# Performance work log

Hardware: AMD Instinct MI355X
Metric: run time of the kernel (lower is better)

Reference implementation:

```python
import jax, jax.numpy as jnp
import numpy as np
import math

# Static config (mirrors init_kwargs)
E, B, S, D, F, HMAX = 8, 4, 1024, 1024, 4096, 8
W = 768                      # active slimmable width (multiple giving integer head_dim)
H = max(1, W * HMAX // D)    # = 6 heads at width 768
HD = W // H                  # = 128
TOPK = 2
EPS = 1e-6


def setup_inputs() -> dict:
    key = jax.random.key(0)
    ks = jax.random.split(key, 14)
    sd = 1.0 / math.sqrt(D)
    sf = 1.0 / math.sqrt(F)
    return {
        "x":  jax.random.normal(ks[0], (B, S, D), jnp.float32),
        "wr": jax.random.normal(ks[1], (D, E), jnp.float32) * sd,
        "qw": jax.random.normal(ks[2], (E, D, D), jnp.float32) * sd,
        "qb": jax.random.normal(ks[3], (E, D), jnp.float32) * sd,
        "kw": jax.random.normal(ks[4], (E, D, D), jnp.float32) * sd,
        "kb": jax.random.normal(ks[5], (E, D), jnp.float32) * sd,
        "vw": jax.random.normal(ks[6], (E, D, D), jnp.float32) * sd,
        "vb": jax.random.normal(ks[7], (E, D), jnp.float32) * sd,
        "ow": jax.random.normal(ks[8], (E, D, D), jnp.float32) * sd,
        "ob": jax.random.normal(ks[9], (E, D), jnp.float32) * sd,
        "w1": jax.random.normal(ks[10], (E, F, D), jnp.float32) * sd,
        "b1": jax.random.normal(ks[11], (E, F), jnp.float32) * sd,
        "w2": jax.random.normal(ks[12], (E, D, F), jnp.float32) * sf,
        "b2": jax.random.normal(ks[13], (E, D), jnp.float32) * sf,
    }


def _slim_linear(x, w, b, in_w, out_w):
    # SlimmableLinear: dynamically slice max-size weight/bias to active widths
    return x @ w[:out_w, :in_w].T + b[:out_w]


def _rms_norm(x):
    # SlimmableExpert._layer_norm: RMS normalization (no mean-subtract, no affine)
    var = jnp.mean(jnp.square(x), axis=-1, keepdims=True)
    return x / jnp.sqrt(var + EPS)


def _expert_fwd(x_s, qw, qb, kw, kb, vw, vb, ow, ob, w1, b1, w2, b2):
    # x_s: [B, S, W]  (already sliced to active width)
    # --- slimmable self-attention at width W ---
    q = _slim_linear(x_s, qw, qb, W, W).reshape(B, S, H, HD).transpose(0, 2, 1, 3)
    k = _slim_linear(x_s, kw, kb, W, W).reshape(B, S, H, HD).transpose(0, 2, 1, 3)
    v = _slim_linear(x_s, vw, vb, W, W).reshape(B, S, H, HD).transpose(0, 2, 1, 3)
    scores = jnp.einsum('bhqd,bhkd->bhqk', q, k) / math.sqrt(HD)   # [B,H,S,S]
    attn = jax.nn.softmax(scores, axis=-1)
    ao = jnp.einsum('bhqk,bhkd->bhqd', attn, v)
    ao = ao.transpose(0, 2, 1, 3).reshape(B, S, W)
    ao = _slim_linear(ao, ow, ob, W, W)
    x1 = _rms_norm(x_s + ao)
    # --- slimmable FFN: W -> F (full) -> W, exact GELU (torch default) ---
    h = jax.nn.gelu(_slim_linear(x1, w1, b1, W, F), approximate=False)
    f = _slim_linear(h, w2, b2, F, W)
    return _rms_norm(x1 + f)   # [B,S,W]


def reference(x, wr, qw, qb, kw, kb, vw, vb, ow, ob, w1, b1, w2, b2):
    # Router: softmax over experts, top-k dispatch with renormalized gates
    logits = jnp.einsum('bsd,de->bse', x, wr)            # [B,S,E]
    probs = jax.nn.softmax(logits, axis=-1)
    topv, topi = jax.lax.top_k(probs, TOPK)              # [B,S,K]
    topv = topv / jnp.sum(topv, axis=-1, keepdims=True)
    bi = jnp.arange(B)[:, None, None]
    si = jnp.arange(S)[None, :, None]
    gate = jnp.zeros((B, S, E), x.dtype).at[bi, si, topi].set(topv)  # sparse gate

    # Slice tokens to active width (width embedding skipped: closest stored
    # width 736 != 768, per source shape-match check)
    x_s = x[..., :W]
    outs = []
    for e in range(E):   # small fixed expert count; bounds peak memory
        outs.append(_expert_fwd(x_s, qw[e], qb[e], kw[e], kb[e], vw[e], vb[e],
                                ow[e], ob[e], w1[e], b1[e], w2[e], b2[e]))
    eo = jnp.stack(outs, axis=0)                          # [E,B,S,W]
    out_w = jnp.einsum('bse,ebsw->bsw', gate, eo)         # gate-weighted combine
    # Zero-pad sliced width back to full model dim (per SlimmableExpert)
    out = jnp.concatenate(
        [out_w, jnp.zeros((B, S, D - W), x.dtype)], axis=-1)
    return out
```

## Files before the change

kernel.cpp:

```cpp
#include <hip/hip_runtime.h>
#include <cstdint>

#define NE 8
#define NB 4
#define NS 1024
#define ND 1024
#define NF 4096
#define NW 768
#define NH 6
#define NHD 128
#define NTOK 4096
#define NBH 24
#define RCAP 10496
#define VSTRIDE ((size_t)NTOK * NW)
#define EPS 1e-6f

typedef unsigned short ush;
typedef __attribute__((ext_vector_type(8))) short short8;
typedef __attribute__((ext_vector_type(4))) float f32x4;
typedef __attribute__((ext_vector_type(4))) unsigned short u16x4;

typedef const __attribute__((address_space(1))) void gvoid_t;
typedef __attribute__((address_space(3))) void lvoid_t;

__device__ __forceinline__ void gload16(const void* g, void* l) {
  __builtin_amdgcn_global_load_lds((gvoid_t*)g, (lvoid_t*)l, 16, 0, 0);
}

__device__ __forceinline__ ush f2b(float f) {
  union { float f; uint32_t u; } x; x.f = f;
  uint32_t r = x.u + 0x7fffu + ((x.u >> 16) & 1u);
  return (ush)(r >> 16);
}
__device__ __forceinline__ float b2f(ush u) {
  union { uint32_t u; float f; } x; x.u = (uint32_t)u << 16;
  return x.f;
}
__device__ __forceinline__ int prefix_sum(const int* __restrict__ c, int n) {
  int s = 0;
#pragma unroll 1
  for (int i = 0; i < n; ++i) s += c[i];
  return s;
}


__global__ __launch_bounds__(256, 4)
void router_kernel(const float* __restrict__ x, const float* __restrict__ wr,
                   float* __restrict__ gate, int* __restrict__ inv) {
  int lane = threadIdx.x & 63, wave = threadIdx.x >> 6;
  int t = blockIdx.x * 4 + wave;
  float acc[NE] = {};
  for (int i = 0; i < 16; ++i) {
    int d = lane + i * 64;
    float xv = x[(size_t)t * ND + d];
    const float* wp = wr + (size_t)d * NE;
    float4 w0 = *(const float4*)wp, w1 = *(const float4*)(wp + 4);
    acc[0] += xv * w0.x; acc[1] += xv * w0.y; acc[2] += xv * w0.z; acc[3] += xv * w0.w;
    acc[4] += xv * w1.x; acc[5] += xv * w1.y; acc[6] += xv * w1.z; acc[7] += xv * w1.w;
  }
#pragma unroll
  for (int e = 0; e < NE; ++e)
    for (int m = 1; m < 64; m <<= 1) acc[e] += __shfl_xor(acc[e], m);
  int i1 = 0; float v1 = acc[0];
#pragma unroll
  for (int e = 1; e < NE; ++e) if (acc[e] > v1) { v1 = acc[e]; i1 = e; }
  int i2 = -1; float v2 = -3.0e38f;
#pragma unroll
  for (int e = 0; e < NE; ++e) if (e != i1 && acc[e] > v2) { v2 = acc[e]; i2 = e; }
  float p2 = __expf(v2 - v1);
  float g1 = 1.0f / (1.0f + p2), g2 = p2 / (1.0f + p2);
  if (lane < NE)
    gate[(size_t)t * NE + lane] = (lane == i1) ? g1 : ((lane == i2) ? g2 : 0.0f);
  if (lane < 2) inv[t * 2 + lane] = -1;
}

__global__ __launch_bounds__(1024, 1)
void build_index(const float* __restrict__ gate, int* __restrict__ cnt64s,
                 int* __restrict__ idx_all, int* __restrict__ inv) {
  int e = blockIdx.x >> 2, b = blockIdx.x & 3;
  int s = threadIdx.x, t = b * 1024 + s;
  bool on = gate[(size_t)t * NE + e] > 0.0f;
  idx_all[(e * 4 + b) * 1024 + s] = (b * 1024) | (int)0x80000000;
  __shared__ int wsum[16], wbase[16];
  unsigned long long mask = __ballot(on);
  int lane = s & 63, wv = s >> 6;
  if (lane == 0) wsum[wv] = __popcll(mask);
  __syncthreads();
  if (s == 0) {
    int acc = 0;
    for (int i = 0; i < 16; ++i) { wbase[i] = acc; acc += wsum[i]; }
    cnt64s[e * 4 + b] = (acc + 63) & ~63;
  }
  __syncthreads();
  if (on) {
    int pos = wbase[wv] + __popcll(mask & ((1ull << lane) - 1ull));
    idx_all[(e * 4 + b) * 1024 + pos] = t;
    int k = 0;
#pragma unroll
    for (int j = 0; j < NE; ++j) k += (j < e && gate[(size_t)t * NE + j] > 0.0f);
    inv[t * 2 + k] = (e << 12) | pos;
  }
}

__global__ __launch_bounds__(256, 4)
void cast_all(const float* __restrict__ x,
              const float* __restrict__ qw, const float* __restrict__ kw,
              const float* __restrict__ vw, const float* __restrict__ ow,
              const float* __restrict__ w1, const float* __restrict__ w2,
              ush* __restrict__ xs,
              ush* __restrict__ dq, ush* __restrict__ dk, ush* __restrict__ dv,
              ush* __restrict__ dwo, ush* __restrict__ d1, ush* __restrict__ d2) {
  int y = blockIdx.y;
  if (y == 8) {
    const int n4 = NTOK * NW / 4;
    for (int u = blockIdx.x * 256 + threadIdx.x; u < n4; u += gridDim.x * 256) {
      int r = u / (NW / 4), c = u - r * (NW / 4);
      float4 v = *(const float4*)(x + (size_t)r * ND + c * 4);
      u16x4 o; o.x = f2b(v.x); o.y = f2b(v.y); o.z = f2b(v.z); o.w = f2b(v.w);
      *(u16x4*)(xs + (size_t)u * 4) = o;
    }
    return;
  }
  const int e = y;
  const int Q4 = 147456;
  const int W14 = 786432;
  const int total = 4 * Q4 + 2 * W14;
  const float* qe = qw + (size_t)e * ND * ND;
  const float* ke = kw + (size_t)e * ND * ND;
  const float* ve = vw + (size_t)e * ND * ND;
  const float* oe = ow + (size_t)e * ND * ND;
  const float* w1e = w1 + (size_t)e * NF * ND;
  const float* w2e = w2 + (size_t)e * ND * NF;
  ush* dqe = dq + (size_t)e * NW * NW;
  ush* dke = dk + (size_t)e * NW * NW;
  ush* dve = dv + (size_t)e * NW * NW;
  ush* doe = dwo + (size_t)e * NW * NW;
  ush* d1e = d1 + (size_t)e * NF * NW;
  ush* d2e = d2 + (size_t)e * NW * NF;
  for (int u = blockIdx.x * 256 + threadIdx.x; u < total; u += gridDim.x * 256) {
    const float* src; ush* dst; int ldsrc, cols4, rel;
    if (u < 4 * Q4) {
      int which = u / Q4; rel = u - which * Q4;
      src = (which == 0) ? qe : (which == 1) ? ke : (which == 2) ? ve : oe;
      dst = (which == 0) ? dqe : (which == 1) ? dke : (which == 2) ? dve : doe;
      ldsrc = 1024; cols4 = 192;
    } else if (u < 4 * Q4 + W14) {
      rel = u - 4 * Q4; src = w1e; dst = d1e; ldsrc = 1024; cols4 = 192;
    } else {
      rel = u - 4 * Q4 - W14; src = w2e; dst = d2e; ldsrc = 4096; cols4 = 1024;
    }
    int r = rel / cols4, c = rel - r * cols4;
    float4 v = *(const float4*)(src + (size_t)r * ldsrc + (size_t)c * 4);
    u16x4 o; o.x = f2b(v.x); o.y = f2b(v.y); o.z = f2b(v.z); o.w = f2b(v.w);
    *(u16x4*)(dst + (size_t)rel * 4) = o;
  }
}

#define BM 128
#define BN 128

__device__ __forceinline__ float gelu_fast(float v) {
  float u = v * fmaf(0.0356774081f, v * v, 0.7978845608f);
  float p = __expf(2.0f * fabsf(u));
  float th = fmaf(-2.0f, __builtin_amdgcn_rcpf(p + 1.0f), 1.0f);
  th = copysignf(th, u);
  return 0.5f * v * (1.0f + th);
}

__device__ __forceinline__ void stage_geom2(int tid, int u, int PAIR, int& row, int& kb) {
  row = u + PAIR * (((tid >> 2) ^ (u >> 2)) & 1);
  kb = ((tid ^ u) & 3) << 4;
}

__global__ __launch_bounds__(256, 3)
void qkv_gemm(const ush* __restrict__ A,
              const ush* __restrict__ wqb, const ush* __restrict__ wkb,
              const ush* __restrict__ wvb,
              const float* __restrict__ qbias, const float* __restrict__ kbias,
              const float* __restrict__ vbias,
              ush* __restrict__ qg, ush* __restrict__ kg, ush* __restrict__ vtg,
              const int* __restrict__ cnt64s, const int* __restrict__ idx_all) {
  const int bid = blockIdx.x;
  const int e = bid & 7, wi = bid >> 3;
  const int bn = wi % 6, bm = (wi / 6) % 32, w = wi / 192;
  int sb = 0, cnt = 0;
  if (w == 0) {
    int sec = e * 4 + (bm >> 3);
    cnt = cnt64s[sec];
    if (((bm & 7) * 128) >= cnt) return;
    sb = prefix_sum(cnt64s, sec);
  }
  const ush* Bw = ((w == 0) ? wqb : (w == 1) ? wkb : wvb) + (size_t)e * NW * NW;
  const float* bias = ((w == 0) ? qbias : (w == 1) ? kbias : vbias) + (size_t)e * ND;

  __shared__ __align__(16) char LDS[3 * 16384];

  const int tid = threadIdx.x, lane = tid & 63, wave = tid >> 6;
  const int lr = lane & 15, lg = lane >> 4;
  const int wr = wave >> 1, wc = wave & 1;

  size_t srcOff[4];
#pragma unroll
  for (int c = 0; c < 4; ++c) {
    int u = (c & 1) * 32 + (tid >> 3), row, kb;
    stage_geom2(tid, u, 64, row, kb);
    int gRow;
    if (c < 2) {
      if (w == 0) {
        int lrow = (bm & 7) * 128 + row;
        gRow = idx_all[(e * 4 + (bm >> 3)) * 1024 + lrow] & 0x7fffffff;
      } else {
        gRow = bm * BM + row;
      }
    } else {
      gRow = bn * BN + row;
    }
    srcOff[c] = (size_t)gRow * (NW * 2) + kb;
  }

  int offA[4], offB[4];
#pragma unroll
  for (int i = 0; i < 4; ++i) {
    offA[i] = (i * 16 + lr) * 128 + (((wr << 6) | (lg << 4)) ^ ((lr & 7) << 4));
    offB[i] = (i * 16 + lr) * 128 + (((wc << 6) | (lg << 4)) ^ ((lr & 7) << 4)) + 8192;
  }

  auto stg = [&](int slot, int kt) {
    size_t kOff = (size_t)kt * 64;
    char* dst = LDS + slot * 16384;
#pragma unroll
    for (int c = 0; c < 4; ++c) {
      const char* src = (c < 2) ? (const char*)A + srcOff[c] + kOff
                                : (const char*)Bw + srcOff[c] + kOff;
      gload16(src, dst + c * 4096 + tid * 16);
    }
  };

  f32x4 acc[4][4] = {};
  const int nkt = NW / 32;
  stg(0, 0); stg(1, 1);
  asm volatile("s_waitcnt vmcnt(4)" ::: "memory");
  asm volatile("s_barrier" ::: "memory");
  int slot = 0;
  for (int kt = 0; kt < nkt; ++kt) {
    int s2 = slot + 2; if (s2 >= 3) s2 -= 3;
    bool more = (kt + 2 < nkt);
    if (more) stg(s2, kt + 2);
    const char* base = LDS + slot * 16384;
    short8 af[4], bfr[4];
#pragma unroll
    for (int i = 0; i < 4; ++i) {
      af[i] = *(const short8*)(base + offA[i]);
      bfr[i] = *(const short8*)(base + offB[i]);
    }
    __builtin_amdgcn_s_setprio(1);
#pragma unroll
    for (int i = 0; i < 4; ++i)
#pragma unroll
      for (int j = 0; j < 4; ++j)
        acc[i][j] = __builtin_amdgcn_mfma_f32_16x16x32_bf16(af[i], bfr[j], acc[i][j], 0, 0, 0);
    __builtin_amdgcn_s_setprio(0);
    if (more) asm volatile("s_waitcnt vmcnt(4)" ::: "memory");
    else      asm volatile("s_waitcnt vmcnt(0)" ::: "memory");
    asm volatile("s_barrier" ::: "memory");
    slot = (slot == 2) ? 0 : slot + 1;
  }

  if (w == 2) {
#pragma unroll
    for (int i = 0; i < 4; ++i) {
      int sl = wr * 64 + i * 16 + lg * 4;
#pragma unroll
      for (int j = 0; j < 4; ++j) {
        int d = wc * 64 + j * 16 + lr;
        float bb = bias[bn * BN + d];
        u16x4 wv_;
#pragma unroll
        for (int r = 0; r < 4; ++r) wv_[r] = f2b(acc[i][j][r] + bb);
        *(u16x4*)(LDS + d * 256 + ((sl * 2) ^ ((d & 15) << 4))) = wv_;
      }
    }
    __syncthreads();
    int d = tid >> 1, sh = (tid & 1) * 64;
    int b_ = bm >> 3, s0b = (bm & 7) * 128;
    ush* gdst = vtg + (size_t)e * VSTRIDE +
                ((size_t)(b_ * NH + bn) * NHD + d) * NS + s0b + sh;
#pragma unroll
    for (int c = 0; c < 8; ++c) {
      short8 v = *(const short8*)(LDS + d * 256 + (((sh + c * 8) * 2) ^ ((d & 15) << 4)));
      *(short8*)(gdst + c * 8) = v;
    }
    return;
  }

#pragma unroll
  for (int i = 0; i < 4; ++i) {
    int lm16 = (bm & 7) * 128 + wr * 64 + i * 16;
    int m0 = bm * BM + wr * 64 + i * 16 + lg * 4;
#pragma unroll
    for (int j = 0; j < 4; ++j) {
      int n = bn * BN + wc * 64 + j * 16 + lr;
      float bb = bias[n];
      if (w == 0) {
        if (lm16 < cnt) {
          int grow = sb + lm16 + lg * 4;
#pragma unroll
          for (int r = 0; r < 4; ++r)
            qg[(size_t)(grow + r) * NW + n] = f2b(acc[i][j][r] + bb);
        }
      } else {
        ush* o = kg + (size_t)e * NTOK * NW;
#pragma unroll
        for (int r = 0; r < 4; ++r)
          o[(size_t)(m0 + r) * NW + n] = f2b(acc[i][j][r] + bb);
      }
    }
  }
}

__global__ __launch_bounds__(256, 3)
void attn2(const ush* __restrict__ Qg, const ush* __restrict__ Kg,
           const ush* __restrict__ VTg, ush* __restrict__ ao,
           const int* __restrict__ cnt64s) {
  const int bid = blockIdx.x;
  const int e = bid & 7, wi = bid >> 3;
  const int qb = wi & 15, bh = wi >> 4;
  const int b = bh / NH, h = bh % NH;
  const int sec = e * 4 + b;
  const int cnt = cnt64s[sec];
  if (qb * 64 >= cnt) return;
  const int sb = prefix_sum(cnt64s, sec);

  __shared__ __align__(16) ush Ks[64 * 128];
  __shared__ __align__(16) ush VTs[128 * 64];
  __shared__ __align__(16) ush Ps[4 * 16 * 64];

  const int tid = threadIdx.x, lane = tid & 63, wave = tid >> 6;
  const int lr = lane & 15, lg = lane >> 4;
  const float cexp = 1.4426950408889634f / sqrtf((float)NHD);

  const ush* Ke = Kg + (size_t)e * NTOK * NW;
  const ush* Ve = VTg + (size_t)e * VSTRIDE;

  int growq = sb + qb * 64 + wave * 16 + lr;
  short8 qf[4];
#pragma unroll
  for (int kk = 0; kk < 4; ++kk)
    qf[kk] = *(const short8*)(Qg + (size_t)growq * NW + h * NHD + kk * 32 + lg * 8);

  f32x4 accv[8] = {};
  float mr[4] = {-3.0e38f, -3.0e38f, -3.0e38f, -3.0e38f};
  float ls[4] = {};

  for (int kt = 0; kt < 16; ++kt) {
    __syncthreads();
#pragma unroll
    for (int p = 0; p < 4; ++p) {
      int o = p * 4096 + tid * 16;
      int row = o >> 8, cb = o & 255;
      gload16((const char*)Ke + ((size_t)(b * NS + kt * 64 + row) * NW + h * NHD) * 2 +
                  (cb ^ ((row & 7) << 4)),
              (char*)Ks + o);
    }
#pragma unroll
    for (int p = 0; p < 4; ++p) {
      int o = p * 4096 + tid * 16;
      int d = o >> 7, cb = o & 127;
      gload16((const char*)Ve + ((size_t)((b * NH + h) * NHD + d) * NS + kt * 64) * 2 +
                  (cb ^ ((d & 7) << 4)),
              (char*)VTs + o);
    }
    __syncthreads();

    f32x4 s[4] = {};
    __builtin_amdgcn_s_setprio(1);
#pragma unroll
    for (int kg2 = 0; kg2 < 4; ++kg2)
#pragma unroll
      for (int kk = 0; kk < 4; ++kk) {
        int row = kg2 * 16 + lr;
        short8 kf = *(const short8*)((const char*)Ks + row * 256 +
                                     ((kk * 64 + lg * 16) ^ ((row & 7) << 4)));
        s[kg2] = __builtin_amdgcn_mfma_f32_16x16x32_bf16(qf[kk], kf, s[kg2], 0, 0, 0);
      }
    __builtin_amdgcn_s_setprio(0);

    float mt[4];
#pragma unroll
    for (int r = 0; r < 4; ++r) {
      float m0 = fmaxf(fmaxf(s[0][r], s[1][r]), fmaxf(s[2][r], s[3][r]));
#pragma unroll
      for (int mm = 1; mm < 16; mm <<= 1) m0 = fmaxf(m0, __shfl_xor(m0, mm));
      mt[r] = m0;
    }
    bool need = (mt[0] > mr[0] + 8.f) || (mt[1] > mr[1] + 8.f) ||
                (mt[2] > mr[2] + 8.f) || (mt[3] > mr[3] + 8.f);
    if (__any(need)) {
#pragma unroll
      for (int r = 0; r < 4; ++r) {
        float mn = fmaxf(mr[r], mt[r]);
        float sc = exp2f((mr[r] - mn) * cexp);
        mr[r] = mn; ls[r] *= sc;
#pragma unroll
        for (int dg = 0; dg < 8; ++dg) accv[dg][r] *= sc;
      }
    }

    char* pw = (char*)Ps + wave * 2048;
#pragma unroll
    for (int kg2 = 0; kg2 < 4; ++kg2)
#pragma unroll
      for (int r = 0; r < 4; ++r) {
        float p = exp2f((s[kg2][r] - mr[r]) * cexp);
        ls[r] += p;
        int row = lg * 4 + r;
        *(ush*)(pw + row * 128 + (((kg2 * 16 + lr) * 2) ^ ((row & 7) << 4))) = f2b(p);
      }
    short8 pf[2];
#pragma unroll
    for (int kk2 = 0; kk2 < 2; ++kk2)
      pf[kk2] = *(const short8*)(pw + lr * 128 + ((kk2 * 64 + lg * 16) ^ ((lr & 7) << 4)));

    __builtin_amdgcn_s_setprio(1);
#pragma unroll
    for (int dg = 0; dg < 8; ++dg) {
      int d = dg * 16 + lr;
#pragma unroll
      for (int kk2 = 0; kk2 < 2; ++kk2) {
        short8 vf = *(const short8*)((const char*)VTs + d * 128 +
                                     ((kk2 * 64 + lg * 16) ^ ((d & 7) << 4)));
        accv[dg] = __builtin_amdgcn_mfma_f32_16x16x32_bf16(pf[kk2], vf, accv[dg], 0, 0, 0);
      }
    }
    __builtin_amdgcn_s_setprio(0);
  }

#pragma unroll
  for (int r = 0; r < 4; ++r)
#pragma unroll
    for (int mm = 1; mm < 16; mm <<= 1) ls[r] += __shfl_xor(ls[r], mm);

#pragma unroll
  for (int r = 0; r < 4; ++r) {
    int growr = sb + qb * 64 + wave * 16 + lg * 4 + r;
    float inv_ = 1.0f / ls[r];
#pragma unroll
    for (int dg = 0; dg < 8; ++dg)
      ao[(size_t)growr * NW + h * NHD + dg * 16 + lr] = f2b(accv[dg][r] * inv_);
  }
}

__global__ __launch_bounds__(256, 2)
void csr_gemm_w(const ush* __restrict__ A, const ush* __restrict__ Ball,
                const float* __restrict__ biasAll, ush* __restrict__ out,
                int N, int Kld, int klen, int nbn,
                int strideBe, int biasStride,
                const int* __restrict__ cnt64s) {
  const int bid = blockIdx.x;
  const int e = bid & 7, wi = bid >> 3;
  const int bn = wi % nbn, bm = wi / nbn;
  const int Re = cnt64s[e * 4] + cnt64s[e * 4 + 1] + cnt64s[e * 4 + 2] + cnt64s[e * 4 + 3];
  if (bm * BM >= Re) return;
  const int ebase = prefix_sum(cnt64s, e * 4);
  const ush* Bw = Ball + (size_t)e * strideBe;
  const float* bias = biasAll + (size_t)e * biasStride;

  __shared__ __align__(16) char LDS[3 * 24576];

  const int tid = threadIdx.x, lane = tid & 63, wave = tid >> 6;
  const int lr = lane & 15, lg = lane >> 4;
  const int wr = wave >> 1, wc = wave & 1;

  size_t srcOff[6];
#pragma unroll
  for (int c = 0; c < 2; ++c) {
    int u = c * 32 + (tid >> 3), row, kb;
    stage_geom2(tid, u, 64, row, kb);
    srcOff[c] = (size_t)(ebase + bm * BM + row) * (Kld * 2) + kb;
  }
#pragma unroll
  for (int c = 0; c < 4; ++c) {
    int u = c * 32 + (tid >> 3), row, kb;
    stage_geom2(tid, u, 128, row, kb);
    srcOff[2 + c] = (size_t)(bn * 256 + row) * (Kld * 2) + kb;
  }

  int offA[4], offB[8];
#pragma unroll
  for (int i = 0; i < 4; ++i)
    offA[i] = (i * 16 + lr) * 128 + (((wr << 6) | (lg << 4)) ^ ((lr & 7) << 4));
#pragma unroll
  for (int j = 0; j < 8; ++j)
    offB[j] = (j * 16 + lr) * 128 + (((wc << 6) | (lg << 4)) ^ ((lr & 7) << 4)) + 8192;

  auto stg = [&](int slot, int kt) {
    size_t kOff = (size_t)kt * 64;
    char* dst = LDS + slot * 24576;
#pragma unroll
    for (int c = 0; c < 2; ++c)
      gload16((const char*)A + srcOff[c] + kOff, dst + c * 4096 + tid * 16);
#pragma unroll
    for (int c = 0; c < 4; ++c)
      gload16((const char*)Bw + srcOff[2 + c] + kOff, dst + 8192 + c * 4096 + tid * 16);
  };

  f32x4 acc[4][8] = {};
  const int nkt = klen / 32;
  stg(0, 0); stg(1, 1);
  asm volatile("s_waitcnt vmcnt(6)" ::: "memory");
  asm volatile("s_barrier" ::: "memory");
  int slot = 0;
  for (int kt = 0; kt < nkt; ++kt) {
    int s2 = slot + 2; if (s2 >= 3) s2 -= 3;
    bool more = (kt + 2 < nkt);
    if (more) stg(s2, kt + 2);
    const char* base = LDS + slot * 24576;
    short8 af[4], bfr[8];
#pragma unroll
    for (int i = 0; i < 4; ++i) af[i] = *(const short8*)(base + offA[i]);
#pragma unroll
    for (int j = 0; j < 8; ++j) bfr[j] = *(const short8*)(base + offB[j]);
    __builtin_amdgcn_s_setprio(1);
#pragma unroll
    for (int i = 0; i < 4; ++i)
#pragma unroll
      for (int j = 0; j < 8; ++j)
        acc[i][j] = __builtin_amdgcn_mfma_f32_16x16x32_bf16(af[i], bfr[j], acc[i][j], 0, 0, 0);
    __builtin_amdgcn_s_setprio(0);
    if (more) asm volatile("s_waitcnt vmcnt(6)" ::: "memory");
    else      asm volatile("s_waitcnt vmcnt(0)" ::: "memory");
    asm volatile("s_barrier" ::: "memory");
    slot = (slot == 2) ? 0 : slot + 1;
  }

#pragma unroll
  for (int i = 0; i < 4; ++i) {
    int lm16 = bm * BM + wr * 64 + i * 16;
    if (lm16 >= Re) continue;
#pragma unroll
    for (int j = 0; j < 8; ++j) {
      int n = bn * 256 + wc * 128 + j * 16 + lr;
      float bb = bias[n];
      int row0 = ebase + lm16 + lg * 4;
#pragma unroll
      for (int r = 0; r < 4; ++r)
        out[(size_t)(row0 + r) * N + n] = f2b(gelu_fast(acc[i][j][r] + bb));
    }
  }
}

__global__ __launch_bounds__(256, 3)
void csr_gemm(const ush* __restrict__ A, const ush* __restrict__ Ball,
              const float* __restrict__ biasAll, ush* __restrict__ out,
              int N, int Kld, int klen, int nbn, int nbm, int nsplit,
              int strideBe, int biasStride,
              const int* __restrict__ cnt64s) {
  const int bid = blockIdx.x;
  const int e = bid & 7, wi = bid >> 3;
  const int bn = wi % nbn, bm = (wi / nbn) % nbm, s = wi / (nbn * nbm);
  const int Re = cnt64s[e * 4] + cnt64s[e * 4 + 1] + cnt64s[e * 4 + 2] + cnt64s[e * 4 + 3];
  if (bm * BM >= Re) return;
  const int ebase = prefix_sum(cnt64s, e * 4);
  const ush* Bw = Ball + (size_t)e * strideBe;
  const float* bias = (s == 0) ? biasAll + (size_t)e * biasStride : nullptr;
  const int koff = s * klen;
  ush* outp = out + (size_t)s * RCAP * N;

  __shared__ __align__(16) char LDS[3 * 16384];

  const int tid = threadIdx.x, lane = tid & 63, wave = tid >> 6;
  const int lr = lane & 15, lg = lane >> 4;
  const int wr = wave >> 1, wc = wave & 1;

  size_t srcOff[4];
#pragma unroll
  for (int c = 0; c < 4; ++c) {
    int u = (c & 1) * 32 + (tid >> 3), row, kb;
    stage_geom2(tid, u, 64, row, kb);
    int gRow = (c < 2) ? (ebase + bm * BM + row) : (bn * BN + row);
    srcOff[c] = (size_t)gRow * (Kld * 2) + (size_t)koff * 2 + kb;
  }

  int offA[4], offB[4];
#pragma unroll
  for (int i = 0; i < 4; ++i) {
    offA[i] = (i * 16 + lr) * 128 + (((wr << 6) | (lg << 4)) ^ ((lr & 7) << 4));
    offB[i] = (i * 16 + lr) * 128 + (((wc << 6) | (lg << 4)) ^ ((lr & 7) << 4)) + 8192;
  }

  auto stg = [&](int slot, int kt) {
    size_t kOff = (size_t)kt * 64;
    char* dst = LDS + slot * 16384;
#pragma unroll
    for (int c = 0; c < 4; ++c) {
      const char* src = (c < 2) ? (const char*)A + srcOff[c] + kOff
                                : (const char*)Bw + srcOff[c] + kOff;
      gload16(src, dst + c * 4096 + tid * 16);
    }
  };

  f32x4 acc[4][4] = {};
  const int nkt = klen / 32;
  stg(0, 0); stg(1, 1);
  asm volatile("s_waitcnt vmcnt(4)" ::: "memory");
  asm volatile("s_barrier" ::: "memory");
  int slot = 0;
  for (int kt = 0; kt < nkt; ++kt) {
    int s2 = slot + 2; if (s2 >= 3) s2 -= 3;
    bool more = (kt + 2 < nkt);
    if (more) stg(s2, kt + 2);
    const char* base = LDS + slot * 16384;
    short8 af[4], bfr[4];
#pragma unroll
    for (int i = 0; i < 4; ++i) {
      af[i] = *(const short8*)(base + offA[i]);
      bfr[i] = *(const short8*)(base + offB[i]);
    }
    __builtin_amdgcn_s_setprio(1);
#pragma unroll
    for (int i = 0; i < 4; ++i)
#pragma unroll
      for (int j = 0; j < 4; ++j)
        acc[i][j] = __builtin_amdgcn_mfma_f32_16x16x32_bf16(af[i], bfr[j], acc[i][j], 0, 0, 0);
    __builtin_amdgcn_s_setprio(0);
    if (more) asm volatile("s_waitcnt vmcnt(4)" ::: "memory");
    else      asm volatile("s_waitcnt vmcnt(0)" ::: "memory");
    asm volatile("s_barrier" ::: "memory");
    slot = (slot == 2) ? 0 : slot + 1;
  }

#pragma unroll
  for (int i = 0; i < 4; ++i) {
    int lm16 = bm * BM + wr * 64 + i * 16;
    if (lm16 >= Re) continue;
#pragma unroll
    for (int j = 0; j < 4; ++j) {
      int n = bn * BN + wc * 64 + j * 16 + lr;
      float bb = bias ? bias[n] : 0.0f;
      int row0 = ebase + lm16 + lg * 4;
#pragma unroll
      for (int r = 0; r < 4; ++r)
        outp[(size_t)(row0 + r) * N + n] = f2b(acc[i][j][r] + bb);
    }
  }
}

__global__ __launch_bounds__(256, 4)
void rmsnorm_res(const float* __restrict__ x, const ush* __restrict__ ooP,
                 ush* __restrict__ x1b, const int* __restrict__ cnt64s,
                 const int* __restrict__ idx_all) {
  int r = blockIdx.x;
  int base = 0, sec = -1, loc = 0;
#pragma unroll 1
  for (int i = 0; i < 32; ++i) {
    int cc = cnt64s[i];
    if (sec < 0 && r < base + cc) { sec = i; loc = r - base; }
    base += cc;
  }
  if (sec < 0) return;
  int t = idx_all[sec * 1024 + loc] & 0x7fffffff;
  __shared__ float red[4];
  int c = threadIdx.x, lane = c & 63, wave = c >> 6;
  float v[3]; float ss = 0.0f;
#pragma unroll
  for (int i = 0; i < 3; ++i) {
    int col = c + i * 256;
    float a = x[(size_t)t * ND + col] + b2f(ooP[(size_t)r * NW + col]);
    v[i] = a; ss += a * a;
  }
#pragma unroll
  for (int m = 1; m < 64; m <<= 1) ss += __shfl_xor(ss, m);
  if (lane == 0) red[wave] = ss;
  __syncthreads();
  float tot = red[0] + red[1] + red[2] + red[3];
  float scale = rsqrtf(tot / (float)NW + EPS);
#pragma unroll
  for (int i = 0; i < 3; ++i) {
    int col = c + i * 256;
    x1b[(size_t)r * NW + col] = f2b(v[i] * scale);
  }
}

__global__ __launch_bounds__(256, 4)
void final_token(const ush* __restrict__ x1b, const ush* __restrict__ ffp,
                 const float* __restrict__ gate, const int* __restrict__ inv,
                 const int* __restrict__ cnt64s, float* __restrict__ out) {
  int t = blockIdx.x, c = threadIdx.x, lane = c & 63, wave = c >> 6;
  __shared__ float red[4];
  float acc[3] = {0.0f, 0.0f, 0.0f};
#pragma unroll 1
  for (int k = 0; k < 2; ++k) {
    int v = inv[t * 2 + k];
    if (v >= 0) {
      int e = v >> 12, pos = v & 0xfff;
      int b = t >> 10;
      int grow = prefix_sum(cnt64s, e * 4 + b) + pos;
      float g = gate[(size_t)t * NE + e];
      float vv[3]; float ss = 0.0f;
#pragma unroll
      for (int i = 0; i < 3; ++i) {
        int col = c + i * 256;
        float f = b2f(ffp[(size_t)grow * NW + col]) +
                  b2f(ffp[(size_t)RCAP * NW + (size_t)grow * NW + col]);
        float a = b2f(x1b[(size_t)grow * NW + col]) + f;
        vv[i] = a; ss += a * a;
      }
#pragma unroll
      for (int m = 1; m < 64; m <<= 1) ss += __shfl_xor(ss, m);
      if (lane == 0) red[wave] = ss;
      __syncthreads();
      float tot = red[0] + red[1] + red[2] + red[3];
      float scale = rsqrtf(tot / (float)NW + EPS) * g;
#pragma unroll
      for (int i = 0; i < 3; ++i) acc[i] += vv[i] * scale;
      __syncthreads();
    }
  }
#pragma unroll
  for (int i = 0; i < 3; ++i) out[(size_t)t * ND + c + i * 256] = acc[i];
  out[(size_t)t * ND + 768 + c] = 0.0f;
}

extern "C" void kernel_launch(void* const* d_in, const int* in_sizes, int n_in,
                              void* d_out, int out_size, void* d_ws, size_t ws_size,
                              hipStream_t stream) {
  (void)in_sizes; (void)n_in; (void)ws_size; (void)out_size;
  const float* x  = (const float*)d_in[0];
  const float* wr = (const float*)d_in[1];
  const float* qw = (const float*)d_in[2];
  const float* qbias = (const float*)d_in[3];
  const float* kw = (const float*)d_in[4];
  const float* kbias = (const float*)d_in[5];
  const float* vw = (const float*)d_in[6];
  const float* vbias = (const float*)d_in[7];
  const float* ow = (const float*)d_in[8];
  const float* obias = (const float*)d_in[9];
  const float* w1 = (const float*)d_in[10];
  const float* b1 = (const float*)d_in[11];
  const float* w2 = (const float*)d_in[12];
  const float* b2 = (const float*)d_in[13];
  float* out = (float*)d_out;
  char* ws = (char*)d_ws;

  size_t off = 0;
  auto alloc = [&](size_t bytes) {
    void* p = ws + off;
    off += (bytes + 255) & ~(size_t)255;
    return p;
  };
  float* gate = (float*)alloc((size_t)NTOK * NE * 4);
  int* cnt64s = (int*)alloc(32 * 4);
  int* idx_all = (int*)alloc((size_t)NE * NTOK * 4);
  int* inv = (int*)alloc((size_t)NTOK * 2 * 4);
  ush* xs  = (ush*)alloc((size_t)NTOK * NW * 2);
  ush* wqb = (ush*)alloc((size_t)NE * NW * NW * 2);
  ush* wkb = (ush*)alloc((size_t)NE * NW * NW * 2);
  ush* wvb = (ush*)alloc((size_t)NE * NW * NW * 2);
  ush* wob = (ush*)alloc((size_t)NE * NW * NW * 2);
  ush* w1b = (ush*)alloc((size_t)NE * NF * NW * 2);
  ush* w2b = (ush*)alloc((size_t)NE * NW * NF * 2);
  ush* x1b = (ush*)alloc((size_t)RCAP * NW * 2);
  char* arena1 = (char*)alloc((size_t)RCAP * NF * 2);
  ush* qg  = (ush*)arena1;
  ush* aog = (ush*)(arena1 + 16121856);
  ush* hb  = (ush*)arena1;
  char* arena2 = (char*)alloc(112852992);
  ush* kg  = (ush*)arena2;
  ush* vtg = (ush*)(arena2 + 50331648);
  ush* ooP = (ush*)(arena2 + 16121856);
  ush* ffp = (ush*)(arena2 + 32243712);

  router_kernel<<<dim3(NTOK / 4), 256, 0, stream>>>(x, wr, gate, inv);
  build_index<<<dim3(NE * NB), 1024, 0, stream>>>(gate, cnt64s, idx_all, inv);
  cast_all<<<dim3(288, 9), 256, 0, stream>>>(x, qw, kw, vw, ow, w1, w2,
                                             xs, wqb, wkb, wvb, wob, w1b, w2b);

  qkv_gemm<<<dim3(8 * 576), 256, 0, stream>>>(
      xs, wqb, wkb, wvb, qbias, kbias, vbias, qg, kg, vtg, cnt64s, idx_all);

  attn2<<<dim3(8 * 384), 256, 0, stream>>>(qg, kg, vtg, aog, cnt64s);

  csr_gemm<<<dim3(8 * 192), 256, 0, stream>>>(
      aog, wob, obias, ooP, NW, NW, NW, 6, 32, 1, NW * NW, ND, cnt64s);

  rmsnorm_res<<<dim3(RCAP), 256, 0, stream>>>(x, ooP, x1b, cnt64s, idx_all);

  csr_gemm_w<<<dim3(8 * 512), 256, 0, stream>>>(
      x1b, w1b, b1, hb, NF, NW, NW, 16, NF * NW, NF, cnt64s);

  csr_gemm<<<dim3(8 * 384), 256, 0, stream>>>(
      hb, w2b, b2, ffp, NW, NF, 2048, 6, 32, 2, NW * NF, ND, cnt64s);

  final_token<<<dim3(NTOK), 256, 0, stream>>>(x1b, ffp, gate, inv, cnt64s, out);
}
```

Measured before the change: 561.4 us.

## Double-buffer K/V tiles in attention kernel to overlap loads with MFMA

```diff
diff --git a/kernel.cpp b/kernel.cpp
--- a/kernel.cpp
+++ b/kernel.cpp
@@ -318,7 +318,7 @@
   }
 }
 
-__global__ __launch_bounds__(256, 3)
+__global__ __launch_bounds__(256, 2)
 void attn2(const ush* __restrict__ Qg, const ush* __restrict__ Kg,
            const ush* __restrict__ VTg, ush* __restrict__ ao,
            const int* __restrict__ cnt64s) {
@@ -331,8 +331,7 @@
   if (qb * 64 >= cnt) return;
   const int sb = prefix_sum(cnt64s, sec);
 
-  __shared__ __align__(16) ush Ks[64 * 128];
-  __shared__ __align__(16) ush VTs[128 * 64];
+  __shared__ __align__(16) char KV[2][32768];
   __shared__ __align__(16) ush Ps[4 * 16 * 64];
 
   const int tid = threadIdx.x, lane = tid & 63, wave = tid >> 6;
@@ -348,29 +347,40 @@
   for (int kk = 0; kk < 4; ++kk)
     qf[kk] = *(const short8*)(Qg + (size_t)growq * NW + h * NHD + kk * 32 + lg * 8);
 
+  int kRow[4], kCb[4], vD[4], vCb[4];
+#pragma unroll
+  for (int p = 0; p < 4; ++p) {
+    int o = p * 4096 + tid * 16;
+    kRow[p] = o >> 8; kCb[p] = (o & 255) ^ ((kRow[p] & 7) << 4);
+    vD[p] = o >> 7;   vCb[p] = (o & 127) ^ ((vD[p] & 7) << 4);
+  }
+
+  auto stg = [&](int slot, int kt) {
+    char* dst = &KV[slot][0];
+#pragma unroll
+    for (int p = 0; p < 4; ++p)
+      gload16((const char*)Ke + ((size_t)(b * NS + kt * 64 + kRow[p]) * NW + h * NHD) * 2 + kCb[p],
+              dst + p * 4096 + tid * 16);
+#pragma unroll
+    for (int p = 0; p < 4; ++p)
+      gload16((const char*)Ve + ((size_t)((b * NH + h) * NHD + vD[p]) * NS + kt * 64) * 2 + vCb[p],
+              dst + 16384 + p * 4096 + tid * 16);
+  };
+
   f32x4 accv[8] = {};
   float mr[4] = {-3.0e38f, -3.0e38f, -3.0e38f, -3.0e38f};
   float ls[4] = {};
 
+  stg(0, 0);
+  asm volatile("s_waitcnt vmcnt(0)" ::: "memory");
+  asm volatile("s_barrier" ::: "memory");
+
   for (int kt = 0; kt < 16; ++kt) {
-    __syncthreads();
-#pragma unroll
-    for (int p = 0; p < 4; ++p) {
-      int o = p * 4096 + tid * 16;
-      int row = o >> 8, cb = o & 255;
-      gload16((const char*)Ke + ((size_t)(b * NS + kt * 64 + row) * NW + h * NHD) * 2 +
-                  (cb ^ ((row & 7) << 4)),
-              (char*)Ks + o);
-    }
-#pragma unroll
-    for (int p = 0; p < 4; ++p) {
-      int o = p * 4096 + tid * 16;
-      int d = o >> 7, cb = o & 127;
-      gload16((const char*)Ve + ((size_t)((b * NH + h) * NHD + d) * NS + kt * 64) * 2 +
-                  (cb ^ ((d & 7) << 4)),
-              (char*)VTs + o);
-    }
-    __syncthreads();
+    const int cur = kt & 1;
+    const bool more = (kt + 1 < 16);
+    if (more) stg(cur ^ 1, kt + 1);
+    const char* Ks = &KV[cur][0];
+    const char* VTs = &KV[cur][16384];
 
     f32x4 s[4] = {};
     __builtin_amdgcn_s_setprio(1);
@@ -379,7 +389,7 @@
 #pragma unroll
       for (int kk = 0; kk < 4; ++kk) {
         int row = kg2 * 16 + lr;
-        short8 kf = *(const short8*)((const char*)Ks + row * 256 +
+        short8 kf = *(const short8*)(Ks + row * 256 +
                                      ((kk * 64 + lg * 16) ^ ((row & 7) << 4)));
         s[kg2] = __builtin_amdgcn_mfma_f32_16x16x32_bf16(qf[kk], kf, s[kg2], 0, 0, 0);
       }
@@ -427,12 +437,15 @@
       int d = dg * 16 + lr;
 #pragma unroll
       for (int kk2 = 0; kk2 < 2; ++kk2) {
-        short8 vf = *(const short8*)((const char*)VTs + d * 128 +
+        short8 vf = *(const short8*)(VTs + d * 128 +
                                      ((kk2 * 64 + lg * 16) ^ ((d & 7) << 4)));
         accv[dg] = __builtin_amdgcn_mfma_f32_16x16x32_bf16(pf[kk2], vf, accv[dg], 0, 0, 0);
       }
     }
     __builtin_amdgcn_s_setprio(0);
+
+    if (more) asm volatile("s_waitcnt vmcnt(0)" ::: "memory");
+    asm volatile("s_barrier" ::: "memory");
   }
 
 #pragma unroll
```

Measured after the change: 574.2 us. 2.3% more time.
